# Kernel optimization log

Hardware: AMD Instinct MI355X
Metric: run time of the kernel (lower is better)

## Reference

```python
import jax, jax.numpy as jnp
from jax import lax
import numpy as np

C_IN, H, W = 9, 11, 11
N_FILT = 64
N_LAYERS = 8
FC_UNITS = 64
LSTM_H = 64
N_ACTIONS = 6
B, T = 32, 128


def setup_inputs() -> dict:
    key = jax.random.key(0)
    ks = jax.random.split(key, 24)
    s = 0.05
    d = {}
    d['x'] = jax.random.normal(ks[0], (B, T, C_IN, H, W), dtype=jnp.float32)
    d['conv0_w'] = jax.random.normal(ks[1], (N_FILT, C_IN, 3, 3), dtype=jnp.float32) * s
    d['conv0_b'] = jnp.zeros((N_FILT,), jnp.float32)
    d['conv_ws'] = jax.random.normal(ks[2], (N_LAYERS - 1, N_FILT, N_FILT, 3, 3), dtype=jnp.float32) * s
    d['conv_bs'] = jnp.zeros((N_LAYERS - 1, N_FILT), jnp.float32)
    d['fc_w'] = jax.random.normal(ks[3], (FC_UNITS, N_FILT * H * W), dtype=jnp.float32) * s
    d['fc_b'] = jnp.zeros((FC_UNITS,), jnp.float32)
    d['w_ih'] = jax.random.normal(ks[4], (4 * LSTM_H, FC_UNITS), dtype=jnp.float32) * s
    d['w_hh'] = jax.random.normal(ks[5], (4 * LSTM_H, LSTM_H), dtype=jnp.float32) * s
    d['b_ih'] = jnp.zeros((4 * LSTM_H,), jnp.float32)
    d['b_hh'] = jnp.zeros((4 * LSTM_H,), jnp.float32)
    d['p1_w'] = jax.random.normal(ks[6], (128, LSTM_H), dtype=jnp.float32) * s
    d['p1_b'] = jnp.zeros((128,), jnp.float32)
    d['p2_w'] = jax.random.normal(ks[7], (N_ACTIONS, 128), dtype=jnp.float32) * s
    d['p2_b'] = jnp.zeros((N_ACTIONS,), jnp.float32)
    d['v1_w'] = jax.random.normal(ks[8], (128, LSTM_H), dtype=jnp.float32) * s
    d['v1_b'] = jnp.zeros((128,), jnp.float32)
    d['v2_w'] = jax.random.normal(ks[9], (1, 128), dtype=jnp.float32) * s
    d['v2_b'] = jnp.zeros((1,), jnp.float32)
    return d


def _conv_relu(h, w, b):
    # h: [N, C, H, W], w: [O, I, 3, 3] -> SAME padding, stride 1
    y = lax.conv_general_dilated(h, w, (1, 1), [(1, 1), (1, 1)],
                                 dimension_numbers=('NCHW', 'OIHW', 'NCHW'))
    return jax.nn.relu(y + b[None, :, None, None])


def _forward(x, conv0_w, conv0_b, conv_ws, conv_bs, fc_w, fc_b,
             w_ih, w_hh, b_ih, b_hh, p1_w, p1_b, p2_w, p2_b, v1_w, v1_b, v2_w, v2_b):
    b, t = x.shape[0], x.shape[1]
    h = x.reshape(b * t, C_IN, H, W)          # batch CNN over all frames at once
    h = _conv_relu(h, conv0_w, conv0_b)
    for i in range(N_LAYERS - 1):             # fixed small layer loop
        h = _conv_relu(h, conv_ws[i], conv_bs[i])
    h = h.reshape(b * t, N_FILT * H * W)
    feats = jax.nn.relu(h @ fc_w.T + fc_b)    # [B*T, FC_UNITS]
    feats = feats.reshape(b, t, FC_UNITS)

    # LSTM (PyTorch gate order i, f, g, o)
    def step(carry, xt):
        hprev, cprev = carry
        g = xt @ w_ih.T + hprev @ w_hh.T + b_ih + b_hh
        i_g, f_g, g_g, o_g = jnp.split(g, 4, axis=-1)
        c = jax.nn.sigmoid(f_g) * cprev + jax.nn.sigmoid(i_g) * jnp.tanh(g_g)
        hn = jax.nn.sigmoid(o_g) * jnp.tanh(c)
        return (hn, c), hn

    h0 = jnp.zeros((b, LSTM_H), feats.dtype)
    c0 = jnp.zeros((b, LSTM_H), feats.dtype)
    _, outs = lax.scan(step, (h0, c0), jnp.swapaxes(feats, 0, 1))  # [T, B, H]
    lstm_out = jnp.swapaxes(outs, 0, 1)       # [B, T, H]

    p = jax.nn.relu(lstm_out @ p1_w.T + p1_b) @ p2_w.T + p2_b  # [B, T, n_actions]
    v = jax.nn.relu(lstm_out @ v1_w.T + v1_b) @ v2_w.T + v2_b  # [B, T, 1]
    return p, v


def reference(x, conv0_w, conv0_b, conv_ws, conv_bs, fc_w, fc_b,
              w_ih, w_hh, b_ih, b_hh, p1_w, p1_b, p2_w, p2_b, v1_w, v1_b, v2_w, v2_b):
    return _forward(x, conv0_w, conv0_b, conv_ws, conv_bs, fc_w, fc_b,
                    w_ih, w_hh, b_ih, b_hh, p1_w, p1_b, p2_w, p2_b,
                    v1_w, v1_b, v2_w, v2_b)
```

## Files before the change

kernel.cpp:

```cpp
#include <hip/hip_runtime.h>
#include <hip/hip_bf16.h>

typedef __attribute__((ext_vector_type(8))) short short8;
typedef __attribute__((ext_vector_type(4))) short short4_t;
typedef __attribute__((ext_vector_type(4))) float floatx4;

#define MFMA_B16(a,b,c) __builtin_amdgcn_mfma_f32_16x16x32_bf16((a),(b),(c),0,0,0)

__device__ __forceinline__ short f2bf(float f) {
    union { __hip_bfloat16 h; short s; } u;
    u.h = __float2bfloat16(f);
    return u.s;
}

union S8U { short4_t h[2]; short8 v; };

#define N_FRAMES 4096
#define C_IN     9
#define POS      121
#define NF       64
#define FC_K     7744
#define ISTR     20
#define FSZ      10816

#define OFF_W0    0
#define OFF_WP    18432
#define OFF_FCP   534528
#define OFF_WIHT  1525760
#define OFF_BSUM  1591296
#define OFF_ACTS  1592320
#define OFF_XG    66079744
#define OFF_HOUT  70274048

__global__ __launch_bounds__(256) void prep_kernel(
    const float* __restrict__ conv0_w, const float* __restrict__ conv_ws,
    const float* __restrict__ w_ih,
    const float* __restrict__ b_ih, const float* __restrict__ b_hh,
    short* __restrict__ w0, short* __restrict__ wpk,
    float* __restrict__ wihT, float* __restrict__ bsum)
{
    int idx = blockIdx.x*256 + threadIdx.x;
    if (idx < 9216) {
        int o9 = idx >> 10; int r = idx & 1023; int o = r >> 4; int ci = r & 15;
        float v = (ci < 9) ? conv0_w[(o*9 + ci)*9 + o9] : 0.f;
        w0[idx] = f2bf(v);
        return;
    }
    idx -= 9216;
    if (idx < 258048) {
        int l = idx / 36864; int r = idx % 36864; int o9 = r >> 12; int rr = r & 4095;
        int o = rr >> 6; int ci = rr & 63;
        wpk[idx] = f2bf(conv_ws[((l*64 + o)*64 + ci)*9 + o9]);
        return;
    }
    idx -= 258048;
    if (idx < 16384) {
        int k = idx >> 8; int g = idx & 255;
        wihT[idx] = w_ih[g*64 + k];
        return;
    }
    idx -= 16384;
    if (idx < 256) bsum[idx] = b_ih[idx] + b_hh[idx];
}

__global__ __launch_bounds__(256) void fc_transpose(
    const float* __restrict__ fc_w, short* __restrict__ fcp)
{
    __shared__ float row[FC_K];
    const int u = blockIdx.x;
    const int tid = threadIdx.x;
    const float* src = fc_w + (size_t)u*FC_K;
    for (int i = tid; i < FC_K; i += 256) row[i] = src[i];
    __syncthreads();
    short* dst = fcp + (size_t)u*FC_K;
    for (int k2 = tid; k2 < FC_K; k2 += 256) {
        int p = k2 >> 6, c = k2 & 63;
        dst[k2] = f2bf(row[c*121 + p]);
    }
}

__global__ __launch_bounds__(256) void conv_stack(
    const float* __restrict__ x,
    const float* __restrict__ conv0_b,
    const float* __restrict__ conv_bs,
    const short* __restrict__ w0,
    const short* __restrict__ wpk,
    short* __restrict__ acts_out)
{
    __shared__ alignas(16) short act[2*FSZ];
    const int tid  = threadIdx.x;
    const int lane = tid & 63;
    const int w    = tid >> 6;
    const int fr   = w >> 1;
    const int mh   = w & 1;
    const int m    = lane & 15;
    const int kg   = lane >> 4;
    const int ht   = tid & 127;
    const int hf   = tid >> 7;

    short* actf = act + fr*FSZ;
    char*  actb = (char*)actf;

    const short8 zero8 = {0,0,0,0,0,0,0,0};
    const floatx4 fzero = {0.f,0.f,0.f,0.f};

    {
        short* ab = act + hf*FSZ;
        for (int i = ht*8; i < 3392; i += 1024) *(short8*)(&ab[i]) = zero8;
    }
    __syncthreads();

    {
        short* ab = act + hf*FSZ;
        const float* xf = x + (size_t)(blockIdx.x*2 + hf)*(C_IN*POS);
        for (int i = ht; i < C_IN*POS; i += 128) {
            int ci = i / POS;
            int p  = i - ci*POS;
            int yy = p / 11;
            int xx = p - yy*11;
            ab[((yy+1)*13 + (xx+1))*ISTR + ci] = f2bf(xf[i]);
        }
    }
    __syncthreads();

    floatx4 acc[2][8];
    #pragma unroll
    for (int mt=0;mt<2;mt++)
        #pragma unroll
        for (int j=0;j<8;j++) acc[mt][j] = fzero;

    int cellA[8], vbase[8];
    #pragma unroll
    for (int j = 0; j < 8; ++j) {
        int p = j*16 + m;
        int pc = (p <= 120) ? p : 120;
        int yy = pc / 11, xx = pc - yy*11;
        cellA[j] = yy*13 + xx;
        vbase[j] = cellA[j]*128;
    }

    {
        const bool kz  = (kg >= 2);
        const int  kgl = (kg & 1)*8;
        const short* w0w = w0 + (mh*32 + m)*16 + kgl;
        #pragma unroll 1
        for (int dy = 0; dy < 3; ++dy) {
            #pragma unroll 1
            for (int dx = 0; dx < 3; ++dx) {
                const short* w9 = w0w + (dy*3+dx)*1024;
                const int so = (dy*13+dx)*ISTR + kgl;
                short8 a[2];
                #pragma unroll
                for (int mt=0;mt<2;mt++) {
                    short8 t = *(const short8*)(w9 + mt*256);
                    a[mt] = kz ? zero8 : t;
                }
                #pragma unroll
                for (int j=0;j<8;j++) {
                    const short* bp = actf + cellA[j]*ISTR + so;
                    S8U t;
                    t.h[0] = *(const short4_t*)(bp);
                    t.h[1] = *(const short4_t*)(bp + 4);
                    short8 b = t.v;
                    #pragma unroll
                    for (int mt=0;mt<2;mt++)
                        acc[mt][j] = MFMA_B16(a[mt], b, acc[mt][j]);
                }
            }
        }
    }

    __syncthreads();
    {
        short* ab = act + hf*FSZ;
        for (int i = ht*8; i < FSZ; i += 1024) *(short8*)(&ab[i]) = zero8;
    }
    __syncthreads();

    auto epilogue = [&](const float* bias) {
        __syncthreads();
        #pragma unroll
        for (int mt=0;mt<2;mt++) {
            const int ch0 = mh*32 + mt*16 + kg*4;
            const int gw  = ch0 >> 3;
            const int off = 1792 + (((gw + m) & 7)<<4) + (kg&1)*8;
            floatx4 bb = *(const floatx4*)(bias + ch0);
            #pragma unroll
            for (int j=0;j<8;j++) {
                floatx4 v = acc[mt][j];
                acc[mt][j] = fzero;
                int p = j*16 + m;
                if (p > 120) continue;
                short4_t sv;
                sv.x = f2bf(fmaxf(v.x + bb.x, 0.f));
                sv.y = f2bf(fmaxf(v.y + bb.y, 0.f));
                sv.z = f2bf(fmaxf(v.z + bb.z, 0.f));
                sv.w = f2bf(fmaxf(v.w + bb.w, 0.f));
                *(short4_t*)(actb + vbase[j] + off) = sv;
            }
        }
        __syncthreads();
    };

    epilogue(conv0_b);

    for (int l = 1; l < 8; ++l) {
        const short* wl = wpk + (l-1)*36864 + (mh*32 + m)*64 + kg*8;
        #pragma unroll 1
        for (int dy = 0; dy < 3; ++dy) {
            #pragma unroll 1
            for (int dx = 0; dx < 3; ++dx) {
                const short* wo = wl + (dy*3+dx)*4096;
                const int sb = (dy*13+dx)*128;
                const int cu = dy*11 + dx + 4 + kg + m;
                #pragma unroll
                for (int kc = 0; kc < 2; ++kc) {
                    short8 a[2];
                    #pragma unroll
                    for (int mt=0;mt<2;mt++)
                        a[mt] = *(const short8*)(wo + mt*1024 + kc*32);
                    const int soff = sb + (((cu + kc*4) & 7)<<4);
                    #pragma unroll
                    for (int j=0;j<8;j++) {
                        short8 b = *(const short8*)(actb + vbase[j] + soff);
                        #pragma unroll
                        for (int mt=0;mt<2;mt++)
                            acc[mt][j] = MFMA_B16(a[mt], b, acc[mt][j]);
                    }
                }
            }
        }
        epilogue(conv_bs + (l-1)*NF);
    }

    {
        const char* ab = (const char*)(act + hf*FSZ);
        short* dst = acts_out + (size_t)(blockIdx.x*2 + hf)*FC_K;
        for (int it = 0; it < 8; ++it) {
            int q = ht + it*128;
            if (q < 968) {
                int p = q >> 3, G = q & 7;
                int yy = p / 11, xx = p - yy*11;
                int cell = (yy+1)*13 + (xx+1);
                int slot = (G + p) & 7;
                short8 v = *(const short8*)(ab + cell*128 + slot*16);
                *(short8*)(dst + q*8) = v;
            }
        }
    }
}

__global__ __launch_bounds__(256) void fc_xg_kernel(
    const short* __restrict__ acts, const short* __restrict__ fcp,
    const float* __restrict__ fc_b, const float* __restrict__ wihT,
    const float* __restrict__ bsum, float* __restrict__ xg)
{
    __shared__ alignas(16) float red[3*64*16];
    __shared__ alignas(16) float fbuf[16*64];
    const int tid  = threadIdx.x;
    const int lane = tid & 63;
    const int w    = tid >> 6;
    const int m    = lane & 15;
    const int kg   = lane >> 4;
    const int bm   = blockIdx.x;

    const floatx4 fzero = {0.f,0.f,0.f,0.f};
    floatx4 acc[4];
    #pragma unroll
    for (int nt=0;nt<4;nt++) acc[nt] = fzero;

    const short* arow = acts + (size_t)(bm*16 + m)*FC_K + kg*8;
    const short* brow = fcp + (size_t)m*FC_K + kg*8;

    for (int kc = w; kc < 242; kc += 4) {
        short8 a = *(const short8*)(arow + kc*32);
        #pragma unroll
        for (int nt=0;nt<4;nt++) {
            short8 b = *(const short8*)(brow + (size_t)nt*16*FC_K + kc*32);
            acc[nt] = MFMA_B16(a, b, acc[nt]);
        }
    }

    if (w > 0) {
        #pragma unroll
        for (int nt=0;nt<4;nt++)
            *(floatx4*)(&red[((w-1)*64 + lane)*16 + nt*4]) = acc[nt];
    }
    __syncthreads();
    if (w == 0) {
        #pragma unroll
        for (int nt=0;nt<4;nt++)
            for (int j=0;j<3;j++)
                acc[nt] += *(const floatx4*)(&red[(j*64 + lane)*16 + nt*4]);
        #pragma unroll
        for (int nt=0;nt<4;nt++) {
            int unit = nt*16 + m;
            float bias = fc_b[unit];
            int fr = kg*4;
            fbuf[(fr+0)*NF + unit] = fmaxf(acc[nt].x + bias, 0.f);
            fbuf[(fr+1)*NF + unit] = fmaxf(acc[nt].y + bias, 0.f);
            fbuf[(fr+2)*NF + unit] = fmaxf(acc[nt].z + bias, 0.f);
            fbuf[(fr+3)*NF + unit] = fmaxf(acc[nt].w + bias, 0.f);
        }
    }
    __syncthreads();

    {
        const int g = tid;
        float a[16];
        float bs = bsum[g];
        #pragma unroll
        for (int i=0;i<16;i++) a[i] = bs;
        for (int k=0;k<64;k++) {
            float wk = wihT[k*256 + g];
            #pragma unroll
            for (int i=0;i<16;i++) a[i] += fbuf[i*64 + k] * wk;
        }
        float* xo = xg + (size_t)(bm*16)*256 + g;
        #pragma unroll
        for (int i=0;i<16;i++) xo[i*256] = a[i];
    }
}

__device__ __forceinline__ float sigmf_(float v){
    return __builtin_amdgcn_rcpf(1.f + __expf(-v));
}
__device__ __forceinline__ float tanhf_(float v){
    return 1.f - 2.f*__builtin_amdgcn_rcpf(__expf(2.f*v) + 1.f);
}

__global__ __launch_bounds__(128) void lstm_kernel(
    const float* __restrict__ xg, const float* __restrict__ whh,
    float* __restrict__ hout)
{
    __shared__ alignas(16) float hbuf[64];
    __shared__ alignas(16) float gbuf[256];
    const int t = threadIdx.x;
    const int b = blockIdx.x;

    float4 w0v[16], w1v[16];
    #pragma unroll
    for (int k=0;k<16;k++) w0v[k] = *(const float4*)(whh + t*64 + k*4);
    #pragma unroll
    for (int k=0;k<16;k++) w1v[k] = *(const float4*)(whh + (t+128)*64 + k*4);

    float c = 0.f;
    if (t < 64) hbuf[t] = 0.f;
    __syncthreads();

    const float* xr = xg + (size_t)(b*128)*256;
    float nA = xr[t];
    float nB = xr[t+128];

    for (int ts=0; ts<128; ++ts) {
        float aA = nA, aB = nB;
        if (ts + 1 < 128) {
            const float* xn = xr + (ts+1)*256;
            nA = xn[t];
            nB = xn[t+128];
        }
        #pragma unroll
        for (int k=0;k<16;k++) {
            float4 hv = *(const float4*)(&hbuf[k*4]);
            aA += hv.x*w0v[k].x + hv.y*w0v[k].y + hv.z*w0v[k].z + hv.w*w0v[k].w;
            aB += hv.x*w1v[k].x + hv.y*w1v[k].y + hv.z*w1v[k].z + hv.w*w1v[k].w;
        }
        gbuf[t] = aA;
        gbuf[t+128] = aB;
        __syncthreads();
        if (t < 64) {
            float ig = sigmf_(gbuf[t]);
            float fg = sigmf_(gbuf[64+t]);
            float gg = tanhf_(gbuf[128+t]);
            float og = sigmf_(gbuf[192+t]);
            c = fg*c + ig*gg;
            float h = og*tanhf_(c);
            hbuf[t] = h;
            hout[(b*128+ts)*64 + t] = h;
        }
        __syncthreads();
    }
}

__global__ __launch_bounds__(64) void heads_kernel(
    const float* __restrict__ hout,
    const float* __restrict__ p1w, const float* __restrict__ p1b,
    const float* __restrict__ p2w, const float* __restrict__ p2b,
    const float* __restrict__ v1w, const float* __restrict__ v1b,
    const float* __restrict__ v2w, const float* __restrict__ v2b,
    float* __restrict__ out)
{
    __shared__ alignas(16) float hbuf[64];
    __shared__ alignas(16) float a1[128];
    __shared__ alignas(16) float a2[128];
    const int lane = threadIdx.x;
    for (int fi=0; fi<4; ++fi) {
        const int f = blockIdx.x*4 + fi;
        hbuf[lane] = hout[f*64 + lane];
        __syncthreads();
        #pragma unroll
        for (int uu=0; uu<2; ++uu) {
            const int u = lane + uu*64;
            float s1 = p1b[u], s2 = v1b[u];
            const float4* wp1 = (const float4*)(p1w + u*64);
            const float4* wv1 = (const float4*)(v1w + u*64);
            #pragma unroll
            for (int k=0;k<16;k++) {
                float4 h4 = *(const float4*)(&hbuf[k*4]);
                float4 w4 = wp1[k];
                s1 += h4.x*w4.x + h4.y*w4.y + h4.z*w4.z + h4.w*w4.w;
                float4 q4 = wv1[k];
                s2 += h4.x*q4.x + h4.y*q4.y + h4.z*q4.z + h4.w*q4.w;
            }
            a1[u] = fmaxf(s1, 0.f);
            a2[u] = fmaxf(s2, 0.f);
        }
        __syncthreads();
        if (lane < 6) {
            float s = p2b[lane];
            const float* wr = p2w + lane*128;
            #pragma unroll
            for (int j=0;j<128;j++) s += a1[j]*wr[j];
            out[f*6 + lane] = s;
        }
        if (lane == 6) {
            float s = v2b[0];
            #pragma unroll
            for (int j=0;j<128;j++) s += a2[j]*v2w[j];
            out[24576 + f] = s;
        }
        __syncthreads();
    }
}

extern "C" void kernel_launch(void* const* d_in, const int* in_sizes, int n_in,
                              void* d_out, int out_size, void* d_ws, size_t ws_size,
                              hipStream_t stream) {
    const float* x       = (const float*)d_in[0];
    const float* conv0_w = (const float*)d_in[1];
    const float* conv0_b = (const float*)d_in[2];
    const float* conv_ws = (const float*)d_in[3];
    const float* conv_bs = (const float*)d_in[4];
    const float* fc_w    = (const float*)d_in[5];
    const float* fc_b    = (const float*)d_in[6];
    const float* w_ih    = (const float*)d_in[7];
    const float* w_hh    = (const float*)d_in[8];
    const float* b_ih    = (const float*)d_in[9];
    const float* b_hh    = (const float*)d_in[10];
    const float* p1_w    = (const float*)d_in[11];
    const float* p1_b    = (const float*)d_in[12];
    const float* p2_w    = (const float*)d_in[13];
    const float* p2_b    = (const float*)d_in[14];
    const float* v1_w    = (const float*)d_in[15];
    const float* v1_b    = (const float*)d_in[16];
    const float* v2_w    = (const float*)d_in[17];
    const float* v2_b    = (const float*)d_in[18];
    float* out = (float*)d_out;

    char* ws = (char*)d_ws;
    short* w0    = (short*)(ws + OFF_W0);
    short* wpk   = (short*)(ws + OFF_WP);
    short* fcp   = (short*)(ws + OFF_FCP);
    float* wihT  = (float*)(ws + OFF_WIHT);
    float* bsum  = (float*)(ws + OFF_BSUM);
    short* acts  = (short*)(ws + OFF_ACTS);
    float* xgb   = (float*)(ws + OFF_XG);
    float* hout  = (float*)(ws + OFF_HOUT);

    prep_kernel<<<1109, 256, 0, stream>>>(conv0_w, conv_ws, w_ih, b_ih, b_hh,
                                          w0, wpk, wihT, bsum);
    fc_transpose<<<64, 256, 0, stream>>>(fc_w, fcp);
    conv_stack<<<N_FRAMES/2, 256, 0, stream>>>(x, conv0_b, conv_bs, w0, wpk, acts);
    fc_xg_kernel<<<256, 256, 0, stream>>>(acts, fcp, fc_b, wihT, bsum, xgb);
    lstm_kernel<<<32, 128, 0, stream>>>(xgb, w_hh, hout);
    heads_kernel<<<1024, 64, 0, stream>>>(hout, p1_w, p1_b, p2_w, p2_b,
                                          v1_w, v1_b, v2_w, v2_b, out);
}
```

Baseline: 560.8 us.

## Run one wave per frame with 32x32x16 MFMA and no block barriers

The conv stack now runs one 64-lane wave per frame instead of two frames across four waves per block. It switches from 16x16x32 to 32x32x16 bf16 MFMA tiles, and the prep kernel repacks the weights to match the new operand layout. Because each frame lives in a single wave, every __syncthreads is removed and each B fragment load is reused across two larger output tiles. The risks are lower latency hiding per block, since there is a single wave and launch bounds of 64 with 2, plus higher register pressure from the floatx16 accumulators.

```diff
diff --git a/kernel.cpp b/kernel.cpp
--- a/kernel.cpp
+++ b/kernel.cpp
@@ -4,8 +4,10 @@
 typedef __attribute__((ext_vector_type(8))) short short8;
 typedef __attribute__((ext_vector_type(4))) short short4_t;
 typedef __attribute__((ext_vector_type(4))) float floatx4;
+typedef __attribute__((ext_vector_type(16))) float floatx16;
 
 #define MFMA_B16(a,b,c) __builtin_amdgcn_mfma_f32_16x16x32_bf16((a),(b),(c),0,0,0)
+#define MFMA32(a,b,c)   __builtin_amdgcn_mfma_f32_32x32x16_bf16((a),(b),(c),0,0,0)
 
 __device__ __forceinline__ short f2bf(float f) {
     union { __hip_bfloat16 h; short s; } u;
@@ -41,16 +43,24 @@
 {
     int idx = blockIdx.x*256 + threadIdx.x;
     if (idx < 9216) {
-        int o9 = idx >> 10; int r = idx & 1023; int o = r >> 4; int ci = r & 15;
-        float v = (ci < 9) ? conv0_w[(o*9 + ci)*9 + o9] : 0.f;
+        int tap = idx >> 10; int r = idx & 1023;
+        int mt = r >> 9; int o = (r >> 4) & 31; int ci = r & 15;
+        int oc = mt*32 + o;
+        float v = (ci < 9) ? conv0_w[(oc*9 + ci)*9 + tap] : 0.f;
         w0[idx] = f2bf(v);
         return;
     }
     idx -= 9216;
     if (idx < 258048) {
-        int l = idx / 36864; int r = idx % 36864; int o9 = r >> 12; int rr = r & 4095;
-        int o = rr >> 6; int ci = rr & 63;
-        wpk[idx] = f2bf(conv_ws[((l*64 + o)*64 + ci)*9 + o9]);
+        int l = idx / 36864; int r = idx % 36864;
+        int tap = r >> 12; int rr = r & 4095;
+        int mt = rr >> 11;
+        int ks = (rr >> 9) & 3;
+        int o  = (rr >> 4) & 31;
+        int ci16 = rr & 15;
+        int oc = mt*32 + o;
+        int ci = ks*16 + ci16;
+        wpk[idx] = f2bf(conv_ws[((l*64 + oc)*64 + ci)*9 + tap]);
         return;
     }
     idx -= 258048;
@@ -79,7 +89,7 @@
     }
 }
 
-__global__ __launch_bounds__(256) void conv_stack(
+__global__ __launch_bounds__(64, 2) void conv_stack(
     const float* __restrict__ x,
     const float* __restrict__ conv0_b,
     const float* __restrict__ conv_bs,
@@ -87,145 +97,119 @@
     const short* __restrict__ wpk,
     short* __restrict__ acts_out)
 {
-    __shared__ alignas(16) short act[2*FSZ];
-    const int tid  = threadIdx.x;
-    const int lane = tid & 63;
-    const int w    = tid >> 6;
-    const int fr   = w >> 1;
-    const int mh   = w & 1;
-    const int m    = lane & 15;
-    const int kg   = lane >> 4;
-    const int ht   = tid & 127;
-    const int hf   = tid >> 7;
-
-    short* actf = act + fr*FSZ;
-    char*  actb = (char*)actf;
+    __shared__ alignas(16) short act[FSZ];
+    const int lane = threadIdx.x;
+    const int n    = lane & 31;
+    const int kh   = lane >> 5;
+    char* actb = (char*)act;
 
     const short8 zero8 = {0,0,0,0,0,0,0,0};
-    const floatx4 fzero = {0.f,0.f,0.f,0.f};
+    const floatx16 fz16 = {};
+
+    for (int i = lane*8; i < 3392; i += 512) *(short8*)(&act[i]) = zero8;
 
     {
-        short* ab = act + hf*FSZ;
-        for (int i = ht*8; i < 3392; i += 1024) *(short8*)(&ab[i]) = zero8;
-    }
-    __syncthreads();
-
-    {
-        short* ab = act + hf*FSZ;
-        const float* xf = x + (size_t)(blockIdx.x*2 + hf)*(C_IN*POS);
-        for (int i = ht; i < C_IN*POS; i += 128) {
+        const float* xf = x + (size_t)blockIdx.x*(C_IN*POS);
+        for (int i = lane; i < C_IN*POS; i += 64) {
             int ci = i / POS;
             int p  = i - ci*POS;
             int yy = p / 11;
             int xx = p - yy*11;
-            ab[((yy+1)*13 + (xx+1))*ISTR + ci] = f2bf(xf[i]);
-        }
-    }
-    __syncthreads();
-
-    floatx4 acc[2][8];
+            act[((yy+1)*13 + (xx+1))*ISTR + ci] = f2bf(xf[i]);
+        }
+    }
+
+    floatx16 acc[2][4];
     #pragma unroll
     for (int mt=0;mt<2;mt++)
         #pragma unroll
-        for (int j=0;j<8;j++) acc[mt][j] = fzero;
-
-    int cellA[8], vbase[8];
+        for (int nt=0;nt<4;nt++) acc[mt][nt] = fz16;
+
+    int cell20[4], vbase[4], wbase[4];
     #pragma unroll
-    for (int j = 0; j < 8; ++j) {
-        int p = j*16 + m;
+    for (int nt = 0; nt < 4; ++nt) {
+        int p = nt*32 + n;
         int pc = (p <= 120) ? p : 120;
         int yy = pc / 11, xx = pc - yy*11;
-        cellA[j] = yy*13 + xx;
-        vbase[j] = cellA[j]*128;
+        int cell = yy*13 + xx;
+        cell20[nt] = cell*ISTR;
+        vbase[nt]  = cell*128;
+        wbase[nt]  = (cell + 14)*128;
     }
 
     {
-        const bool kz  = (kg >= 2);
-        const int  kgl = (kg & 1)*8;
-        const short* w0w = w0 + (mh*32 + m)*16 + kgl;
+        const short* w0l = w0 + n*16 + kh*8;
         #pragma unroll 1
         for (int dy = 0; dy < 3; ++dy) {
             #pragma unroll 1
             for (int dx = 0; dx < 3; ++dx) {
-                const short* w9 = w0w + (dy*3+dx)*1024;
-                const int so = (dy*13+dx)*ISTR + kgl;
-                short8 a[2];
+                const short* wt = w0l + (dy*3+dx)*1024;
+                short8 a0 = *(const short8*)(wt);
+                short8 a1 = *(const short8*)(wt + 512);
+                const int so = (dy*13+dx)*ISTR + kh*8;
                 #pragma unroll
-                for (int mt=0;mt<2;mt++) {
-                    short8 t = *(const short8*)(w9 + mt*256);
-                    a[mt] = kz ? zero8 : t;
-                }
-                #pragma unroll
-                for (int j=0;j<8;j++) {
-                    const short* bp = actf + cellA[j]*ISTR + so;
+                for (int nt=0;nt<4;nt++) {
+                    const short* bp = act + cell20[nt] + so;
                     S8U t;
                     t.h[0] = *(const short4_t*)(bp);
                     t.h[1] = *(const short4_t*)(bp + 4);
-                    short8 b = t.v;
-                    #pragma unroll
-                    for (int mt=0;mt<2;mt++)
-                        acc[mt][j] = MFMA_B16(a[mt], b, acc[mt][j]);
+                    acc[0][nt] = MFMA32(a0, t.v, acc[0][nt]);
+                    acc[1][nt] = MFMA32(a1, t.v, acc[1][nt]);
                 }
             }
         }
     }
 
-    __syncthreads();
-    {
-        short* ab = act + hf*FSZ;
-        for (int i = ht*8; i < FSZ; i += 1024) *(short8*)(&ab[i]) = zero8;
-    }
-    __syncthreads();
+    for (int i = lane*8; i < FSZ; i += 512) *(short8*)(&act[i]) = zero8;
 
     auto epilogue = [&](const float* bias) {
-        __syncthreads();
         #pragma unroll
         for (int mt=0;mt<2;mt++) {
-            const int ch0 = mh*32 + mt*16 + kg*4;
-            const int gw  = ch0 >> 3;
-            const int off = 1792 + (((gw + m) & 7)<<4) + (kg&1)*8;
-            floatx4 bb = *(const floatx4*)(bias + ch0);
-            #pragma unroll
-            for (int j=0;j<8;j++) {
-                floatx4 v = acc[mt][j];
-                acc[mt][j] = fzero;
-                int p = j*16 + m;
-                if (p > 120) continue;
-                short4_t sv;
-                sv.x = f2bf(fmaxf(v.x + bb.x, 0.f));
-                sv.y = f2bf(fmaxf(v.y + bb.y, 0.f));
-                sv.z = f2bf(fmaxf(v.z + bb.z, 0.f));
-                sv.w = f2bf(fmaxf(v.w + bb.w, 0.f));
-                *(short4_t*)(actb + vbase[j] + off) = sv;
+            #pragma unroll
+            for (int q=0;q<4;q++) {
+                const int ch0 = mt*32 + q*8 + kh*4;
+                const floatx4 bb = *(const floatx4*)(bias + ch0);
+                const int soff = (((mt*4 + q + n) & 7) << 4) + kh*8;
+                #pragma unroll
+                for (int nt=0;nt<4;nt++) {
+                    if (nt == 3 && n > 24) continue;
+                    short4_t sv;
+                    sv.x = f2bf(fmaxf(acc[mt][nt][q*4+0] + bb.x, 0.f));
+                    sv.y = f2bf(fmaxf(acc[mt][nt][q*4+1] + bb.y, 0.f));
+                    sv.z = f2bf(fmaxf(acc[mt][nt][q*4+2] + bb.z, 0.f));
+                    sv.w = f2bf(fmaxf(acc[mt][nt][q*4+3] + bb.w, 0.f));
+                    *(short4_t*)(actb + wbase[nt] + soff) = sv;
+                }
             }
         }
-        __syncthreads();
+        #pragma unroll
+        for (int mt=0;mt<2;mt++)
+            #pragma unroll
+            for (int nt=0;nt<4;nt++) acc[mt][nt] = fz16;
     };
 
     epilogue(conv0_b);
 
+    #pragma unroll 1
     for (int l = 1; l < 8; ++l) {
-        const short* wl = wpk + (l-1)*36864 + (mh*32 + m)*64 + kg*8;
+        const short* wl = wpk + (l-1)*36864 + n*16 + kh*8;
         #pragma unroll 1
         for (int dy = 0; dy < 3; ++dy) {
             #pragma unroll 1
             for (int dx = 0; dx < 3; ++dx) {
-                const short* wo = wl + (dy*3+dx)*4096;
+                const short* wt = wl + (dy*3+dx)*4096;
                 const int sb = (dy*13+dx)*128;
-                const int cu = dy*11 + dx + 4 + kg + m;
+                const int cu = dy*11 + dx + 4 + kh + n;
                 #pragma unroll
-                for (int kc = 0; kc < 2; ++kc) {
-                    short8 a[2];
+                for (int ks = 0; ks < 4; ++ks) {
+                    short8 a0 = *(const short8*)(wt + ks*512);
+                    short8 a1 = *(const short8*)(wt + 2048 + ks*512);
+                    const int soff = sb + (((cu + ks*2) & 7) << 4);
                     #pragma unroll
-                    for (int mt=0;mt<2;mt++)
-                        a[mt] = *(const short8*)(wo + mt*1024 + kc*32);
-                    const int soff = sb + (((cu + kc*4) & 7)<<4);
-                    #pragma unroll
-                    for (int j=0;j<8;j++) {
-                        short8 b = *(const short8*)(actb + vbase[j] + soff);
-                        #pragma unroll
-                        for (int mt=0;mt<2;mt++)
-                            acc[mt][j] = MFMA_B16(a[mt], b, acc[mt][j]);
+                    for (int nt=0;nt<4;nt++) {
+                        short8 b = *(const short8*)(actb + vbase[nt] + soff);
+                        acc[0][nt] = MFMA32(a0, b, acc[0][nt]);
+                        acc[1][nt] = MFMA32(a1, b, acc[1][nt]);
                     }
                 }
             }
@@ -234,16 +218,16 @@
     }
 
     {
-        const char* ab = (const char*)(act + hf*FSZ);
-        short* dst = acts_out + (size_t)(blockIdx.x*2 + hf)*FC_K;
-        for (int it = 0; it < 8; ++it) {
-            int q = ht + it*128;
+        short* dst = acts_out + (size_t)blockIdx.x*FC_K;
+        #pragma unroll 1
+        for (int it = 0; it < 16; ++it) {
+            int q = it*64 + lane;
             if (q < 968) {
                 int p = q >> 3, G = q & 7;
                 int yy = p / 11, xx = p - yy*11;
                 int cell = (yy+1)*13 + (xx+1);
                 int slot = (G + p) & 7;
-                short8 v = *(const short8*)(ab + cell*128 + slot*16);
+                short8 v = *(const short8*)(actb + cell*128 + slot*16);
                 *(short8*)(dst + q*8) = v;
             }
         }
@@ -470,7 +454,7 @@
     prep_kernel<<<1109, 256, 0, stream>>>(conv0_w, conv_ws, w_ih, b_ih, b_hh,
                                           w0, wpk, wihT, bsum);
     fc_transpose<<<64, 256, 0, stream>>>(fc_w, fcp);
-    conv_stack<<<N_FRAMES/2, 256, 0, stream>>>(x, conv0_b, conv_bs, w0, wpk, acts);
+    conv_stack<<<N_FRAMES, 64, 0, stream>>>(x, conv0_b, conv_bs, w0, wpk, acts);
     fc_xg_kernel<<<256, 256, 0, stream>>>(acts, fcp, fc_b, wihT, bsum, xgb);
     lstm_kernel<<<32, 128, 0, stream>>>(xgb, w_hh, hout);
     heads_kernel<<<1024, 64, 0, stream>>>(hout, p1_w, p1_b, p2_w, p2_b,
```

After: 549.2 us. -2.1%, faster.
